# Performance work log

Hardware: AMD Instinct MI355X
Metric: run time of the kernel (lower is better)

The kernel has to match this reference:

```python
import jax, jax.numpy as jnp
import numpy as np

K = 3          # kernel_size
S = 2          # stride
NEW = 2        # new_size = int(ratio * stride)
C = 32         # channels
BN_EPS = 1e-5


def _unfold(x, oh, ow):
    # torch.nn.Unfold(K, dilation=1, padding=(K-1)//2, stride=S) reshaped to
    # [B, C, K, K, oh, ow] (channel slowest, then kernel rows, kernel cols).
    p = (K - 1) // 2
    xp = jnp.pad(x, ((0, 0), (0, 0), (p, p), (p, p)))
    rows = []
    for i in range(K):
        cols = []
        for j in range(K):
            cols.append(xp[:, :, i:i + S * (oh - 1) + 1:S, j:j + S * (ow - 1) + 1:S])
        rows.append(jnp.stack(cols, axis=2))          # [B,C,K,oh,ow]
    return jnp.stack(rows, axis=2)                    # [B,C,K,K,oh,ow]


def reference(x, conv_w, bn_gamma, bn_beta, bn_mean, bn_var):
    B, _, W, H = x.shape
    oh = -(-W // S)
    ow = -(-H // S)
    patches = _unfold(x, oh, ow)                      # [B,C,K,K,oh,ow]

    # three max reductions over different unfolded axes
    x1 = patches.max(axis=1).reshape(B, K * K, oh, ow)    # over channels
    x2 = patches.max(axis=2).reshape(B, C * K, oh, ow)    # over kernel rows
    x3 = patches.max(axis=3).reshape(B, C * K, oh, ow)    # over kernel cols
    feat = jnp.concatenate([x1, x2, x3], axis=1)          # [B, K*K+2*C*K, oh, ow]

    # ConvModule: 1x1 conv (no bias, since BN) -> BN (eval stats) -> ReLU
    y = jnp.einsum('bihw,oi->bohw', feat, conv_w)
    inv = (bn_gamma / jnp.sqrt(bn_var + BN_EPS))[None, :, None, None]
    y = (y - bn_mean[None, :, None, None]) * inv + bn_beta[None, :, None, None]
    y = jax.nn.relu(y)

    # dynamic kernel: [B, C, K*K, NEW, NEW, oh, ow]
    w = y.reshape(B, C, K * K, NEW, NEW, oh, ow)
    px = patches.reshape(B, C, K * K, 1, 1, oh, ow)
    out = jnp.mean(px * w, axis=2)                    # [B,C,NEW,NEW,oh,ow]
    out = out.transpose(0, 1, 4, 2, 5, 3)             # [B,C,oh,NEW,ow,NEW]
    out = out.reshape(B, C, oh * NEW, ow * NEW)
    return out[:, :, :W, :H]


def setup_inputs() -> dict:
    key = jax.random.key(0)
    k1, k2 = jax.random.split(key)
    B, W, H = 8, 128, 128
    in_ch = K * C * 2 + K * K                         # 201
    out_ch = C * NEW * NEW * K * K                    # 1152
    x = jax.random.normal(k1, (B, C, W, H), dtype=jnp.float32)
    conv_w = jax.random.normal(k2, (out_ch, in_ch), dtype=jnp.float32) * 0.02
    return {
        'x': x,
        'conv_w': conv_w,
        'bn_gamma': jnp.ones((out_ch,), jnp.float32),
        'bn_beta': jnp.zeros((out_ch,), jnp.float32),
        'bn_mean': jnp.zeros((out_ch,), jnp.float32),
        'bn_var': jnp.ones((out_ch,), jnp.float32),
    }
```

## Files before the change

### kernel.cpp

```cpp
#include <hip/hip_runtime.h>
#include <math.h>

typedef __bf16 v8bf __attribute__((ext_vector_type(8)));
typedef float  v4f  __attribute__((ext_vector_type(4)));

constexpr int Bsz  = 8;
constexpr int Cch  = 32;
constexpr int WIMG = 128;
constexpr int OH   = 64;
constexpr int OW   = 64;
constexpr int INCH = 201;
constexpr int KP   = 224;
constexpr int NK   = 7;
constexpr int OUTCH = 1152;
constexpr int MTOT = Bsz * OH * OW;
constexpr float BN_EPS = 1e-5f;

constexpr size_t WT_BYTES = (size_t)NK * OUTCH * 32 * 2;
constexpr size_t BIAS_OFF = WT_BYTES;
constexpr size_t FEAT_OFF = BIAS_OFF + OUTCH * 4;

typedef const void __attribute__((address_space(1)))* gas_ptr;
typedef void __attribute__((address_space(3)))* las_ptr;
__device__ __forceinline__ void load16_lds(const void* g, void* l) {
    __builtin_amdgcn_global_load_lds((gas_ptr)(uintptr_t)g, (las_ptr)(uintptr_t)l, 16, 0, 0);
}

constexpr int SXS = 132;
constexpr int FEAT_BLOCKS = Bsz * OH;
constexpr int NPREP = OUTCH * KP + OUTCH;
constexpr int PREP_BLOCKS = (NPREP + 255) / 256;

__global__ __launch_bounds__(256)
void prep_feat_kernel(const float* __restrict__ x,
                      const float* __restrict__ conv_w,
                      const float* __restrict__ gamma,
                      const float* __restrict__ beta,
                      const float* __restrict__ mean,
                      const float* __restrict__ var,
                      __bf16* __restrict__ Wt,
                      float* __restrict__ biasp,
                      __bf16* __restrict__ feat) {
    __shared__ __align__(16) float sx[Cch * 3 * SXS];
    __shared__ __align__(16) float cmax[3 * SXS];
    __shared__ __align__(16) __bf16 sfeat[NK * OW * 32];

    const int t = threadIdx.x;

    if (blockIdx.x >= FEAT_BLOCKS) {
        int idx = ((int)blockIdx.x - FEAT_BLOCKS) * 256 + t;
        const int nW = OUTCH * KP;
        if (idx < nW) {
            int o = idx / KP;
            int f = idx - o * KP;
            float inv = gamma[o] * rsqrtf(var[o] + BN_EPS);
            float v = (f < INCH) ? conv_w[o * INCH + f] * inv : 0.0f;
            Wt[((size_t)(f >> 5) * OUTCH + o) * 32 + (f & 31)] = (__bf16)v;
        } else if (idx < nW + OUTCH) {
            int o = idx - nW;
            float inv = gamma[o] * rsqrtf(var[o] + BN_EPS);
            biasp[o] = beta[o] - mean[o] * inv;
        }
        return;
    }

    const int b  = blockIdx.x >> 6;
    const int ho = blockIdx.x & 63;

    for (int idx = t; idx < Cch * 3 * 32; idx += 256) {
        int c   = idx / 96;
        int rem = idx - c * 96;
        int i   = rem >> 5;
        int q   = rem & 31;
        int r   = 2 * ho - 1 + i;
        float4 v = make_float4(0.f, 0.f, 0.f, 0.f);
        if (r >= 0 && r < WIMG)
            v = *(const float4*)(x + (((size_t)(b * Cch + c) * WIMG) + r) * WIMG + q * 4);
        float* dst = sx + (c * 3 + i) * SXS + q * 4 + 1;
        dst[0] = v.x; dst[1] = v.y; dst[2] = v.z; dst[3] = v.w;
    }
    if (t < 96) {
        float* row = sx + t * SXS;
        row[0] = 0.0f; row[129] = 0.0f; row[130] = 0.0f; row[131] = 0.0f;
    }
    __syncthreads();

    if (t < 99) {
        int i = t / 33, cg = t - i * 33;
        const float4* base = (const float4*)sx + i * (SXS / 4) + cg;
        float4 m = base[0];
        #pragma unroll 4
        for (int c = 1; c < Cch; ++c) {
            float4 v = base[(size_t)c * (3 * SXS / 4)];
            m.x = fmaxf(m.x, v.x); m.y = fmaxf(m.y, v.y);
            m.z = fmaxf(m.z, v.z); m.w = fmaxf(m.w, v.w);
        }
        ((float4*)cmax)[i * (SXS / 4) + cg] = m;
    }
    __syncthreads();

    for (int idx = t; idx < 9 * 64; idx += 256) {
        int f = idx >> 6, wo = idx & 63;
        int i = f / 3, j = f - 3 * i;
        sfeat[wo * 32 + f] = (__bf16)cmax[i * SXS + 2 * wo + j];
    }
    {
        const int wp = t & 31, g = t >> 5;
        const int wo0 = 2 * wp;
        #pragma unroll
        for (int cl = 0; cl < 4; ++cl) {
            int c = g * 4 + cl;
            float v[3][5];
            #pragma unroll
            for (int i = 0; i < 3; ++i) {
                const float* row = sx + (c * 3 + i) * SXS + 4 * wp;
                float4 q = *(const float4*)row;
                v[i][0] = q.x; v[i][1] = q.y; v[i][2] = q.z; v[i][3] = q.w;
                v[i][4] = row[4];
            }
            #pragma unroll
            for (int i = 0; i < 3; ++i) {
                int f = 105 + c * 3 + i;
                float a0 = fmaxf(fmaxf(v[i][0], v[i][1]), v[i][2]);
                float a1 = fmaxf(fmaxf(v[i][2], v[i][3]), v[i][4]);
                sfeat[(f >> 5) * 2048 + wo0 * 32 + (f & 31)]       = (__bf16)a0;
                sfeat[(f >> 5) * 2048 + (wo0 + 1) * 32 + (f & 31)] = (__bf16)a1;
            }
            #pragma unroll
            for (int j = 0; j < 3; ++j) {
                int f = 9 + c * 3 + j;
                float a0 = fmaxf(fmaxf(v[0][j], v[1][j]), v[2][j]);
                float a1 = fmaxf(fmaxf(v[0][j + 2], v[1][j + 2]), v[2][j + 2]);
                sfeat[(f >> 5) * 2048 + wo0 * 32 + (f & 31)]       = (__bf16)a0;
                sfeat[(f >> 5) * 2048 + (wo0 + 1) * 32 + (f & 31)] = (__bf16)a1;
            }
        }
    }
    for (int idx = t; idx < 64 * 23; idx += 256) {
        int wo = idx / 23, fo = idx - wo * 23;
        int f = 201 + fo;
        sfeat[6 * 2048 + wo * 32 + (f & 31)] = (__bf16)0.0f;
    }
    __syncthreads();

    const size_t spat0 = (size_t)(b * OH + ho) * OW;
    #pragma unroll
    for (int kc = 0; kc < NK; ++kc) {
        float4 vv = ((const float4*)sfeat)[kc * 256 + t];
        ((float4*)((char*)feat + ((size_t)kc * MTOT + spat0) * 64))[t] = vv;
    }
}

constexpr int YS  = 148;
constexpr int REG = 16 * YS;
__global__ __launch_bounds__(256, 2)
void gemm_kernel(const __bf16* __restrict__ feat,
                 const __bf16* __restrict__ Wt,
                 const float* __restrict__ biasp,
                 const float* __restrict__ x,
                 float* __restrict__ out) {
    __shared__ __align__(16) unsigned char lds[51200];

    const int t    = threadIdx.x;
    const int nb   = (int)blockIdx.x >> 7;
    const int mb   = (int)blockIdx.x & 127;
    const int M0   = mb * 256;
    const int N0   = nb * 144;
    const int wave = t >> 6, lane = t & 63, quad = lane >> 4, l16 = lane & 15;

    auto issue = [&](int ks, int buf) {
        const char* Ag = (const char*)feat + ((size_t)ks * MTOT + M0) * 64;
        char* Ab = (char*)lds + buf * 16384;
        #pragma unroll
        for (int i = 0; i < 4; ++i) {
            int off = (wave * 4 + i) * 1024 + lane * 16;
            load16_lds(Ag + off, Ab + off);
        }
        const char* Bg = (const char*)Wt + ((size_t)ks * OUTCH + N0) * 64;
        char* Bb = (char*)lds + 32768 + buf * 9216;
        #pragma unroll
        for (int i = 0; i < 2; ++i) {
            int off = (wave * 2 + i) * 1024 + lane * 16;
            load16_lds(Bg + off, Bb + off);
        }
        if (wave == 0) {
            int off2 = 8192 + lane * 16;
            load16_lds(Bg + off2, Bb + off2);
        }
    };

    v4f acc[4][9];
    #pragma unroll
    for (int mt = 0; mt < 4; ++mt)
        #pragma unroll
        for (int nt = 0; nt < 9; ++nt)
            acc[mt][nt] = (v4f){0.f, 0.f, 0.f, 0.f};

    issue(0, 0);
    __syncthreads();

    for (int ks = 0; ks < NK; ++ks) {
        const int cur = ks & 1;
        if (ks + 1 < NK) issue(ks + 1, cur ^ 1);

        const char* Ab = (const char*)lds + cur * 16384;
        const char* Bb = (const char*)lds + 32768 + cur * 9216;
        v8bf af[4];
        #pragma unroll
        for (int mt = 0; mt < 4; ++mt)
            af[mt] = *(const v8bf*)(Ab + (wave * 64 + mt * 16 + l16) * 64 + quad * 16);
        #pragma unroll
        for (int nt = 0; nt < 9; ++nt) {
            v8bf bf = *(const v8bf*)(Bb + (nt * 16 + l16) * 64 + quad * 16);
            #pragma unroll
            for (int mt = 0; mt < 4; ++mt)
                acc[mt][nt] = __builtin_amdgcn_mfma_f32_16x16x32_bf16(
                    af[mt], bf, acc[mt][nt], 0, 0, 0);
        }
        __syncthreads();
    }

    float bia[9];
    #pragma unroll
    for (int nt = 0; nt < 9; ++nt) bia[nt] = biasp[N0 + nt * 16 + l16];

    float* yw = (float*)lds + wave * REG;
    const int cl  = lane >> 4;
    const int wl  = lane & 15;
    const int cg  = nb * 4 + cl;
    const float s9 = 1.0f / 9.0f;

    #pragma unroll
    for (int p = 0; p < 4; ++p) {
        #pragma unroll
        for (int nt = 0; nt < 9; ++nt)
            #pragma unroll
            for (int r = 0; r < 4; ++r)
                yw[(quad * 4 + r) * YS + nt * 16 + l16] =
                    fmaxf(acc[p][nt][r] + bia[nt], 0.0f);

        const int mg  = M0 + wave * 64 + p * 16 + wl;
        const int bb  = mg >> 12;
        const int hob = (mg >> 6) & 63;
        const int wo  = mg & 63;
        const float* xc = x + (size_t)(bb * Cch + cg) * WIMG * WIMG;

        float pt[9];
        #pragma unroll
        for (int qi = 0; qi < 3; ++qi) {
            int r = 2 * hob - 1 + qi;
            #pragma unroll
            for (int qj = 0; qj < 3; ++qj) {
                int col = 2 * wo - 1 + qj;
                float v = 0.0f;
                if (r >= 0 && r < WIMG && col >= 0 && col < WIMG)
                    v = xc[r * WIMG + col];
                pt[qi * 3 + qj] = v;
            }
        }
        const float4* yrow = (const float4*)(yw + wl * YS + cl * 36);
        float o00 = 0.f, o01 = 0.f, o10 = 0.f, o11 = 0.f;
        #pragma unroll
        for (int q = 0; q < 9; ++q) {
            float4 yv = yrow[q];
            float pq = pt[q];
            o00 = fmaf(pq, yv.x, o00);
            o01 = fmaf(pq, yv.y, o01);
            o10 = fmaf(pq, yv.z, o10);
            o11 = fmaf(pq, yv.w, o11);
        }
        size_t obase = (((size_t)(bb * Cch + cg) * WIMG) + 2 * hob) * WIMG + 2 * wo;
        *(float2*)(out + obase)        = make_float2(o00 * s9, o01 * s9);
        *(float2*)(out + obase + WIMG) = make_float2(o10 * s9, o11 * s9);
    }
}

extern "C" void kernel_launch(void* const* d_in, const int* in_sizes, int n_in,
                              void* d_out, int out_size, void* d_ws, size_t ws_size,
                              hipStream_t stream) {
    const float* x      = (const float*)d_in[0];
    const float* conv_w = (const float*)d_in[1];
    const float* gamma  = (const float*)d_in[2];
    const float* beta   = (const float*)d_in[3];
    const float* mean   = (const float*)d_in[4];
    const float* var    = (const float*)d_in[5];
    float* out = (float*)d_out;

    __bf16* Wt    = (__bf16*)d_ws;
    float*  biasp = (float*)((char*)d_ws + BIAS_OFF);
    __bf16* feat  = (__bf16*)((char*)d_ws + FEAT_OFF);

    prep_feat_kernel<<<FEAT_BLOCKS + PREP_BLOCKS, 256, 0, stream>>>(
        x, conv_w, gamma, beta, mean, var, Wt, biasp, feat);
    gemm_kernel<<<(OUTCH / 144) * (MTOT / 256), 256, 0, stream>>>(feat, Wt, biasp, x, out);
}
```

Baseline: 119.4 us.

## Fuse prep and GEMM into one cooperative persistent kernel with grid sync

```diff
diff --git a/kernel.cpp b/kernel.cpp
--- a/kernel.cpp
+++ b/kernel.cpp
@@ -1,5 +1,8 @@
 #include <hip/hip_runtime.h>
+#include <hip/hip_cooperative_groups.h>
 #include <math.h>
+
+namespace cg = cooperative_groups;
 
 typedef __bf16 v8bf __attribute__((ext_vector_type(8)));
 typedef float  v4f  __attribute__((ext_vector_type(4)));
@@ -30,6 +33,261 @@
 constexpr int FEAT_BLOCKS = Bsz * OH;
 constexpr int NPREP = OUTCH * KP + OUTCH;
 constexpr int PREP_BLOCKS = (NPREP + 255) / 256;
+
+constexpr int SX_OFF    = 0;
+constexpr int CMAX_OFF  = 50688;
+constexpr int SFEAT_OFF = 52272;
+constexpr int LDS_BYTES = 80944;
+constexpr int YS  = 148;
+constexpr int REG = 16 * YS;
+
+__global__ __launch_bounds__(256, 2)
+void fused_kernel(const float* __restrict__ x,
+                  const float* __restrict__ conv_w,
+                  const float* __restrict__ gamma,
+                  const float* __restrict__ beta,
+                  const float* __restrict__ mean,
+                  const float* __restrict__ var,
+                  __bf16* __restrict__ Wt,
+                  float* __restrict__ biasp,
+                  __bf16* __restrict__ feat,
+                  float* __restrict__ out) {
+    __shared__ __align__(16) unsigned char lds[LDS_BYTES];
+
+    const int t   = threadIdx.x;
+    const int bid = (int)blockIdx.x;
+
+    {
+        const int nW = OUTCH * KP;
+        for (int idx = bid * 256 + t; idx < NPREP; idx += 512 * 256) {
+            if (idx < nW) {
+                int o = idx / KP;
+                int f = idx - o * KP;
+                float inv = gamma[o] * rsqrtf(var[o] + BN_EPS);
+                float v = (f < INCH) ? conv_w[o * INCH + f] * inv : 0.0f;
+                Wt[((size_t)(f >> 5) * OUTCH + o) * 32 + (f & 31)] = (__bf16)v;
+            } else {
+                int o = idx - nW;
+                float inv = gamma[o] * rsqrtf(var[o] + BN_EPS);
+                biasp[o] = beta[o] - mean[o] * inv;
+            }
+        }
+    }
+
+    {
+        float*  sx    = (float*)(lds + SX_OFF);
+        float*  cmax  = (float*)(lds + CMAX_OFF);
+        __bf16* sfeat = (__bf16*)(lds + SFEAT_OFF);
+
+        const int b  = bid >> 6;
+        const int ho = bid & 63;
+
+        for (int idx = t; idx < Cch * 3 * 32; idx += 256) {
+            int c   = idx / 96;
+            int rem = idx - c * 96;
+            int i   = rem >> 5;
+            int q   = rem & 31;
+            int r   = 2 * ho - 1 + i;
+            float4 v = make_float4(0.f, 0.f, 0.f, 0.f);
+            if (r >= 0 && r < WIMG)
+                v = *(const float4*)(x + (((size_t)(b * Cch + c) * WIMG) + r) * WIMG + q * 4);
+            float* dst = sx + (c * 3 + i) * SXS + q * 4 + 1;
+            dst[0] = v.x; dst[1] = v.y; dst[2] = v.z; dst[3] = v.w;
+        }
+        if (t < 96) {
+            float* row = sx + t * SXS;
+            row[0] = 0.0f; row[129] = 0.0f; row[130] = 0.0f; row[131] = 0.0f;
+        }
+        __syncthreads();
+
+        if (t < 99) {
+            int i = t / 33, cg2 = t - i * 33;
+            const float4* base = (const float4*)sx + i * (SXS / 4) + cg2;
+            float4 m = base[0];
+            #pragma unroll 4
+            for (int c = 1; c < Cch; ++c) {
+                float4 v = base[(size_t)c * (3 * SXS / 4)];
+                m.x = fmaxf(m.x, v.x); m.y = fmaxf(m.y, v.y);
+                m.z = fmaxf(m.z, v.z); m.w = fmaxf(m.w, v.w);
+            }
+            ((float4*)cmax)[i * (SXS / 4) + cg2] = m;
+        }
+        __syncthreads();
+
+        for (int idx = t; idx < 9 * 64; idx += 256) {
+            int f = idx >> 6, wo = idx & 63;
+            int i = f / 3, j = f - 3 * i;
+            sfeat[wo * 32 + f] = (__bf16)cmax[i * SXS + 2 * wo + j];
+        }
+        {
+            const int wp = t & 31, g = t >> 5;
+            const int wo0 = 2 * wp;
+            #pragma unroll
+            for (int cl = 0; cl < 4; ++cl) {
+                int c = g * 4 + cl;
+                float v[3][5];
+                #pragma unroll
+                for (int i = 0; i < 3; ++i) {
+                    const float* row = sx + (c * 3 + i) * SXS + 4 * wp;
+                    float4 q = *(const float4*)row;
+                    v[i][0] = q.x; v[i][1] = q.y; v[i][2] = q.z; v[i][3] = q.w;
+                    v[i][4] = row[4];
+                }
+                #pragma unroll
+                for (int i = 0; i < 3; ++i) {
+                    int f = 105 + c * 3 + i;
+                    float a0 = fmaxf(fmaxf(v[i][0], v[i][1]), v[i][2]);
+                    float a1 = fmaxf(fmaxf(v[i][2], v[i][3]), v[i][4]);
+                    sfeat[(f >> 5) * 2048 + wo0 * 32 + (f & 31)]       = (__bf16)a0;
+                    sfeat[(f >> 5) * 2048 + (wo0 + 1) * 32 + (f & 31)] = (__bf16)a1;
+                }
+                #pragma unroll
+                for (int j = 0; j < 3; ++j) {
+                    int f = 9 + c * 3 + j;
+                    float a0 = fmaxf(fmaxf(v[0][j], v[1][j]), v[2][j]);
+                    float a1 = fmaxf(fmaxf(v[0][j + 2], v[1][j + 2]), v[2][j + 2]);
+                    sfeat[(f >> 5) * 2048 + wo0 * 32 + (f & 31)]       = (__bf16)a0;
+                    sfeat[(f >> 5) * 2048 + (wo0 + 1) * 32 + (f & 31)] = (__bf16)a1;
+                }
+            }
+        }
+        for (int idx = t; idx < 64 * 23; idx += 256) {
+            int wo = idx / 23, fo = idx - wo * 23;
+            int f = 201 + fo;
+            sfeat[6 * 2048 + wo * 32 + (f & 31)] = (__bf16)0.0f;
+        }
+        __syncthreads();
+
+        const size_t spat0 = (size_t)(b * OH + ho) * OW;
+        #pragma unroll
+        for (int kc = 0; kc < NK; ++kc) {
+            float4 vv = ((const float4*)sfeat)[kc * 256 + t];
+            ((float4*)((char*)feat + ((size_t)kc * MTOT + spat0) * 64))[t] = vv;
+        }
+    }
+
+    __threadfence();
+    cg::this_grid().sync();
+    __threadfence();
+
+    const int wave = t >> 6, lane = t & 63, quad = lane >> 4, l16 = lane & 15;
+
+    #pragma unroll 1
+    for (int tile = 0; tile < 2; ++tile) {
+        const int tg = bid + tile * 512;
+        const int nb = tg >> 7;
+        const int mb = tg & 127;
+        const int M0 = mb * 256;
+        const int N0 = nb * 144;
+
+        auto issue = [&](int ks, int buf) {
+            const char* Ag = (const char*)feat + ((size_t)ks * MTOT + M0) * 64;
+            char* Ab = (char*)lds + buf * 16384;
+            #pragma unroll
+            for (int i = 0; i < 4; ++i) {
+                int off = (wave * 4 + i) * 1024 + lane * 16;
+                load16_lds(Ag + off, Ab + off);
+            }
+            const char* Bg = (const char*)Wt + ((size_t)ks * OUTCH + N0) * 64;
+            char* Bb = (char*)lds + 32768 + buf * 9216;
+            #pragma unroll
+            for (int i = 0; i < 2; ++i) {
+                int off = (wave * 2 + i) * 1024 + lane * 16;
+                load16_lds(Bg + off, Bb + off);
+            }
+            if (wave == 0) {
+                int off2 = 8192 + lane * 16;
+                load16_lds(Bg + off2, Bb + off2);
+            }
+        };
+
+        v4f acc[4][9];
+        #pragma unroll
+        for (int mt = 0; mt < 4; ++mt)
+            #pragma unroll
+            for (int nt = 0; nt < 9; ++nt)
+                acc[mt][nt] = (v4f){0.f, 0.f, 0.f, 0.f};
+
+        issue(0, 0);
+        __syncthreads();
+
+        for (int ks = 0; ks < NK; ++ks) {
+            const int cur = ks & 1;
+            if (ks + 1 < NK) issue(ks + 1, cur ^ 1);
+
+            const char* Ab = (const char*)lds + cur * 16384;
+            const char* Bb = (const char*)lds + 32768 + cur * 9216;
+            v8bf af[4];
+            #pragma unroll
+            for (int mt = 0; mt < 4; ++mt)
+                af[mt] = *(const v8bf*)(Ab + (wave * 64 + mt * 16 + l16) * 64 + quad * 16);
+            #pragma unroll
+            for (int nt = 0; nt < 9; ++nt) {
+                v8bf bf = *(const v8bf*)(Bb + (nt * 16 + l16) * 64 + quad * 16);
+                #pragma unroll
+                for (int mt = 0; mt < 4; ++mt)
+                    acc[mt][nt] = __builtin_amdgcn_mfma_f32_16x16x32_bf16(
+                        af[mt], bf, acc[mt][nt], 0, 0, 0);
+            }
+            __syncthreads();
+        }
+
+        float bia[9];
+        #pragma unroll
+        for (int nt = 0; nt < 9; ++nt) bia[nt] = biasp[N0 + nt * 16 + l16];
+
+        float* yw = (float*)lds + wave * REG;
+        const int cl  = lane >> 4;
+        const int wl  = lane & 15;
+        const int cg2 = nb * 4 + cl;
+        const float s9 = 1.0f / 9.0f;
+
+        #pragma unroll
+        for (int p = 0; p < 4; ++p) {
+            #pragma unroll
+            for (int nt = 0; nt < 9; ++nt)
+                #pragma unroll
+                for (int r = 0; r < 4; ++r)
+                    yw[(quad * 4 + r) * YS + nt * 16 + l16] =
+                        fmaxf(acc[p][nt][r] + bia[nt], 0.0f);
+
+            const int mg  = M0 + wave * 64 + p * 16 + wl;
+            const int bb  = mg >> 12;
+            const int hob = (mg >> 6) & 63;
+            const int wo  = mg & 63;
+            const float* xc = x + (size_t)(bb * Cch + cg2) * WIMG * WIMG;
+
+            float pt[9];
+            #pragma unroll
+            for (int qi = 0; qi < 3; ++qi) {
+                int r = 2 * hob - 1 + qi;
+                #pragma unroll
+                for (int qj = 0; qj < 3; ++qj) {
+                    int col = 2 * wo - 1 + qj;
+                    float v = 0.0f;
+                    if (r >= 0 && r < WIMG && col >= 0 && col < WIMG)
+                        v = xc[r * WIMG + col];
+                    pt[qi * 3 + qj] = v;
+                }
+            }
+            const float4* yrow = (const float4*)(yw + wl * YS + cl * 36);
+            float o00 = 0.f, o01 = 0.f, o10 = 0.f, o11 = 0.f;
+            #pragma unroll
+            for (int q = 0; q < 9; ++q) {
+                float4 yv = yrow[q];
+                float pq = pt[q];
+                o00 = fmaf(pq, yv.x, o00);
+                o01 = fmaf(pq, yv.y, o01);
+                o10 = fmaf(pq, yv.z, o10);
+                o11 = fmaf(pq, yv.w, o11);
+            }
+            size_t obase = (((size_t)(bb * Cch + cg2) * WIMG) + 2 * hob) * WIMG + 2 * wo;
+            *(float2*)(out + obase)        = make_float2(o00 * s9, o01 * s9);
+            *(float2*)(out + obase + WIMG) = make_float2(o10 * s9, o11 * s9);
+        }
+        __syncthreads();
+    }
+}
 
 __global__ __launch_bounds__(256)
 void prep_feat_kernel(const float* __restrict__ x,
@@ -86,8 +344,8 @@
     __syncthreads();
 
     if (t < 99) {
-        int i = t / 33, cg = t - i * 33;
-        const float4* base = (const float4*)sx + i * (SXS / 4) + cg;
+        int i = t / 33, cg2 = t - i * 33;
+        const float4* base = (const float4*)sx + i * (SXS / 4) + cg2;
         float4 m = base[0];
         #pragma unroll 4
         for (int c = 1; c < Cch; ++c) {
@@ -95,7 +353,7 @@
             m.x = fmaxf(m.x, v.x); m.y = fmaxf(m.y, v.y);
             m.z = fmaxf(m.z, v.z); m.w = fmaxf(m.w, v.w);
         }
-        ((float4*)cmax)[i * (SXS / 4) + cg] = m;
+        ((float4*)cmax)[i * (SXS / 4) + cg2] = m;
     }
     __syncthreads();
 
@@ -151,8 +409,6 @@
     }
 }
 
-constexpr int YS  = 148;
-constexpr int REG = 16 * YS;
 __global__ __launch_bounds__(256, 2)
 void gemm_kernel(const __bf16* __restrict__ feat,
                  const __bf16* __restrict__ Wt,
@@ -227,7 +483,7 @@
     float* yw = (float*)lds + wave * REG;
     const int cl  = lane >> 4;
     const int wl  = lane & 15;
-    const int cg  = nb * 4 + cl;
+    const int cg2 = nb * 4 + cl;
     const float s9 = 1.0f / 9.0f;
 
     #pragma unroll
@@ -243,7 +499,7 @@
         const int bb  = mg >> 12;
         const int hob = (mg >> 6) & 63;
         const int wo  = mg & 63;
-        const float* xc = x + (size_t)(bb * Cch + cg) * WIMG * WIMG;
+        const float* xc = x + (size_t)(bb * Cch + cg2) * WIMG * WIMG;
 
         float pt[9];
         #pragma unroll
@@ -269,7 +525,7 @@
             o10 = fmaf(pq, yv.z, o10);
             o11 = fmaf(pq, yv.w, o11);
         }
-        size_t obase = (((size_t)(bb * Cch + cg) * WIMG) + 2 * hob) * WIMG + 2 * wo;
+        size_t obase = (((size_t)(bb * Cch + cg2) * WIMG) + 2 * hob) * WIMG + 2 * wo;
         *(float2*)(out + obase)        = make_float2(o00 * s9, o01 * s9);
         *(float2*)(out + obase + WIMG) = make_float2(o10 * s9, o11 * s9);
     }
@@ -290,7 +546,16 @@
     float*  biasp = (float*)((char*)d_ws + BIAS_OFF);
     __bf16* feat  = (__bf16*)((char*)d_ws + FEAT_OFF);
 
-    prep_feat_kernel<<<FEAT_BLOCKS + PREP_BLOCKS, 256, 0, stream>>>(
-        x, conv_w, gamma, beta, mean, var, Wt, biasp, feat);
-    gemm_kernel<<<(OUTCH / 144) * (MTOT / 256), 256, 0, stream>>>(feat, Wt, biasp, x, out);
+    void* args[] = {(void*)&x, (void*)&conv_w, (void*)&gamma, (void*)&beta,
+                    (void*)&mean, (void*)&var, (void*)&Wt, (void*)&biasp,
+                    (void*)&feat, (void*)&out};
+    hipError_t e = hipLaunchCooperativeKernel((void*)fused_kernel,
+                                              dim3(512), dim3(256),
+                                              args, 0, stream);
+    if (e != hipSuccess) {
+        (void)hipGetLastError();
+        prep_feat_kernel<<<FEAT_BLOCKS + PREP_BLOCKS, 256, 0, stream>>>(
+            x, conv_w, gamma, beta, mean, var, Wt, biasp, feat);
+        gemm_kernel<<<(OUTCH / 144) * (MTOT / 256), 256, 0, stream>>>(feat, Wt, biasp, x, out);
+    }
 }
```

Measured after the change: 307.1 us. 157% more time.
